# Kernel optimization log

Hardware: AMD Instinct MI355X
Metric: run time of the kernel (lower is better)

## Reference

```python
import jax, jax.numpy as jnp
import numpy as np

B, S, E, H = 1, 4096, 768, 12
D = E // H  # head_dim = 64


def setup_inputs() -> dict:
    key = jax.random.key(0)
    ks = jax.random.split(key, 6)
    scale = 0.02
    x = jax.random.normal(ks[0], (B, S, E), dtype=jnp.float32)
    Wq = jax.random.normal(ks[1], (E, E), dtype=jnp.float32) * scale
    Wk = jax.random.normal(ks[2], (E, E), dtype=jnp.float32) * scale
    Wv = jax.random.normal(ks[3], (E, E), dtype=jnp.float32) * scale
    Wo = jax.random.normal(ks[4], (E, E), dtype=jnp.float32) * scale
    bo = jax.random.normal(ks[5], (E,), dtype=jnp.float32) * scale
    mask = jnp.tril(jnp.ones((S, S), dtype=bool))[None, None]  # [1,1,S,S] causal
    return {"x": x, "Wq": Wq, "Wk": Wk, "Wv": Wv, "Wo": Wo, "bo": bo, "mask": mask}


def reference(x, Wq, Wk, Wv, Wo, bo, mask):
    # projections (torch Linear: y = x @ W.T; here W stored as [E,E] applied as x@W)
    q = jnp.einsum('bse,ef->bsf', x, Wq).reshape(B, S, H, D).transpose(0, 2, 1, 3)
    k = jnp.einsum('bse,ef->bsf', x, Wk).reshape(B, S, H, D).transpose(0, 2, 1, 3)
    v = jnp.einsum('bse,ef->bsf', x, Wv).reshape(B, S, H, D).transpose(0, 2, 1, 3)
    scores = jnp.einsum('bhqd,bhkd->bhqk', q, k) / jnp.sqrt(jnp.float32(D))
    scores = jnp.where(mask, scores, -jnp.inf)
    attn = jax.nn.softmax(scores, axis=-1)  # dropout p=0 -> identity
    ctx = jnp.einsum('bhqk,bhkd->bhqd', attn, v)
    ctx = ctx.transpose(0, 2, 1, 3).reshape(B, S, E)
    return jnp.einsum('bse,ef->bsf', ctx, Wo) + bo
```

## Files before the change

### kernel.cpp

```cpp
#include <hip/hip_runtime.h>
#include <math.h>

#define S 4096
#define E 768
#define H 12
#define Dh 64
#define SCALE2 0.1803368801111204f

typedef short short8 __attribute__((ext_vector_type(8)));
typedef float floatx4 __attribute__((ext_vector_type(4)));

__device__ __forceinline__ unsigned short f2bf(float f) {
    union { float f; unsigned int i; } c; c.f = f;
    unsigned int i = c.i;
    return (unsigned short)((i + 0x7fffu + ((i >> 16) & 1u)) >> 16);
}

__device__ __forceinline__ unsigned int pk_bf16(float lo, float hi) {
#if __has_builtin(__builtin_amdgcn_cvt_pk_bf16_f32)
    typedef __bf16 bf16x2 __attribute__((ext_vector_type(2)));
    union { bf16x2 v; unsigned int u; } c;
    c.v = __builtin_amdgcn_cvt_pk_bf16_f32(lo, hi);
    return c.u;
#else
    union { float f; unsigned int i; } a, b; a.f = lo; b.f = hi;
    return ((a.i + 0x8000u) >> 16) | ((b.i + 0x8000u) & 0xFFFF0000u);
#endif
}

__device__ __forceinline__ void gload_lds16(const unsigned short* g, unsigned short* l) {
    __builtin_amdgcn_global_load_lds(
        (const __attribute__((address_space(1))) unsigned int*)g,
        (__attribute__((address_space(3))) unsigned int*)l, 16, 0, 0);
}

__global__ __launch_bounds__(256)
void prep_kernel(const float* __restrict__ x, unsigned short* __restrict__ xb,
                 const float* __restrict__ s0, const float* __restrict__ s1,
                 const float* __restrict__ s2, const float* __restrict__ s3,
                 unsigned short* __restrict__ d0, unsigned short* __restrict__ d1,
                 unsigned short* __restrict__ d2, unsigned short* __restrict__ d3,
                 float* __restrict__ zbase) {
    __shared__ unsigned short tile[32][33];
    const int b = blockIdx.x;
    const int tid = threadIdx.x;
    if (b < 2304) {
        int z = b / 576, rem = b - z * 576;
        int bx = rem % 24, by = rem / 24;
        const float* src = (z == 0) ? s0 : (z == 1) ? s1 : (z == 2) ? s2 : s3;
        unsigned short* dst = (z == 0) ? d0 : (z == 1) ? d1 : (z == 2) ? d2 : d3;
        int tx = tid & 31, ty = tid >> 5;
        int xcol = bx * 32 + tx;
        int y0 = by * 32;
        for (int j = ty; j < 32; j += 8)
            tile[j][tx] = f2bf(src[(size_t)(y0 + j) * E + xcol]);
        __syncthreads();
        int x2 = y0 + tx;
        int y2 = bx * 32;
        for (int j = ty; j < 32; j += 8)
            dst[(size_t)(y2 + j) * E + x2] = tile[tx][j];
    } else if (b < 3840) {
        int i = ((b - 2304) * 256 + tid) * 8;
        float4 f0 = *reinterpret_cast<const float4*>(x + i);
        float4 f1 = *reinterpret_cast<const float4*>(x + i + 4);
        unsigned short u[8];
        u[0]=f2bf(f0.x); u[1]=f2bf(f0.y); u[2]=f2bf(f0.z); u[3]=f2bf(f0.w);
        u[4]=f2bf(f1.x); u[5]=f2bf(f1.y); u[6]=f2bf(f1.z); u[7]=f2bf(f1.w);
        *reinterpret_cast<uint4*>(xb + i) = *reinterpret_cast<uint4*>(u);
    } else {
        size_t i = ((size_t)(b - 3840) * 256 + tid) * 16;
        float4 z4 = make_float4(0.f, 0.f, 0.f, 0.f);
        *reinterpret_cast<float4*>(zbase + i)      = z4;
        *reinterpret_cast<float4*>(zbase + i + 4)  = z4;
        *reinterpret_cast<float4*>(zbase + i + 8)  = z4;
        *reinterpret_cast<float4*>(zbase + i + 12) = z4;
    }
}

__global__ __launch_bounds__(256)
void gemm_qkv(const unsigned short* __restrict__ A,
              const unsigned short* __restrict__ BT,
              unsigned short* __restrict__ Qb, unsigned short* __restrict__ Kb,
              unsigned short* __restrict__ VTb) {
    __shared__ unsigned short Asm[128 * 64];
    __shared__ unsigned short Bsm[128 * 64];
    const int tid  = threadIdx.x;
    const int wave = tid >> 6, lane = tid & 63;
    const int quad = lane >> 4, l16 = lane & 15;
    const int lrow = lane >> 3, lchunk = lane & 7;
    const int bb = blockIdx.x;
    const int xcd = bb & 7, j = bb >> 3;
    const int mt = (xcd >> 1) * 8 + (j & 7);
    const int nt = (xcd & 1) * 9 + (j >> 3);
    const int n0 = nt * 128;
    const int m0 = mt * 128;
    const int aw = wave >> 1, bw = wave & 1;

    floatx4 acc[4][4];
    #pragma unroll
    for (int at = 0; at < 4; at++)
        #pragma unroll
        for (int ct = 0; ct < 4; ct++)
            #pragma unroll
            for (int r = 0; r < 4; r++) acc[at][ct][r] = 0.f;

    for (int k0 = 0; k0 < E; k0 += 64) {
        #pragma unroll
        for (int i = 0; i < 4; i++) {
            int rbase = wave * 32 + i * 8;
            int row   = rbase + lrow;
            int gc    = lchunk ^ (row & 7);
            gload_lds16(&A [(size_t)(m0 + row) * E + k0 + gc * 8], &Asm[rbase * 64]);
            gload_lds16(&BT[(size_t)(n0 + row) * E + k0 + gc * 8], &Bsm[rbase * 64]);
        }
        __syncthreads();
        #pragma unroll
        for (int kk = 0; kk < 2; kk++) {
            const int g = kk * 4 + quad;
            short8 af[4], bfr[4];
            #pragma unroll
            for (int t = 0; t < 4; t++) {
                int ar = aw * 64 + t * 16 + l16;
                af[t]  = *reinterpret_cast<const short8*>(&Asm[ar * 64 + (g ^ (ar & 7)) * 8]);
                int br = bw * 64 + t * 16 + l16;
                bfr[t] = *reinterpret_cast<const short8*>(&Bsm[br * 64 + (g ^ (br & 7)) * 8]);
            }
            #pragma unroll
            for (int at = 0; at < 4; at++)
                #pragma unroll
                for (int ct = 0; ct < 4; ct++)
                    acc[at][ct] = __builtin_amdgcn_mfma_f32_16x16x32_bf16(af[at], bfr[ct], acc[at][ct], 0, 0, 0);
        }
        __syncthreads();
    }

    const int sec = n0 / 768;
    const int nb  = n0 - sec * 768 + bw * 64;
    #pragma unroll
    for (int at = 0; at < 4; at++)
        #pragma unroll
        for (int ct = 0; ct < 4; ct++) {
            int nsec = nb + ct * 16 + l16, hh = nsec >> 6, d = nsec & 63;
            #pragma unroll
            for (int r = 0; r < 4; r++) {
                int s = m0 + aw * 64 + at * 16 + quad * 4 + r;
                float v = acc[at][ct][r];
                if (sec == 0)      Qb [(size_t)hh * S * Dh + (size_t)s * Dh + d] = f2bf(v * SCALE2);
                else if (sec == 1) Kb [(size_t)hh * S * Dh + (size_t)s * Dh + d] = f2bf(v);
                else               VTb[(size_t)hh * Dh * S + (size_t)d * S + s]  = f2bf(v);
            }
        }
}

__global__ __launch_bounds__(256)
void normctx(const float* __restrict__ ctxf, const float* __restrict__ lsumf,
             unsigned short* __restrict__ ctxb) {
    int i = (blockIdx.x * 256 + threadIdx.x) * 8;
    int s = i / E, e = i - s * E;
    float linv = 1.0f / lsumf[(e >> 6) * S + s];
    float4 f0 = *reinterpret_cast<const float4*>(ctxf + i);
    float4 f1 = *reinterpret_cast<const float4*>(ctxf + i + 4);
    uint4 w;
    w.x = pk_bf16(f0.x * linv, f0.y * linv);
    w.y = pk_bf16(f0.z * linv, f0.w * linv);
    w.z = pk_bf16(f1.x * linv, f1.y * linv);
    w.w = pk_bf16(f1.z * linv, f1.w * linv);
    *reinterpret_cast<uint4*>(ctxb + i) = w;
}

__global__ __launch_bounds__(256)
void gemm_out(const unsigned short* __restrict__ A,
              const unsigned short* __restrict__ BT,
              float* __restrict__ outp, const float* __restrict__ bias) {
    __shared__ unsigned short Asm[128 * 64];
    __shared__ unsigned short Bsm[64 * 64];
    const int tid  = threadIdx.x;
    const int wave = tid >> 6, lane = tid & 63;
    const int quad = lane >> 4, l16 = lane & 15;
    const int lrow = lane >> 3, lchunk = lane & 7;
    const int bb = blockIdx.x;
    const int xcd = bb & 7, j = bb >> 3;
    const int mt = (xcd >> 1) * 8 + (j & 7);
    const int nt = (xcd & 1) * 6 + (j >> 3);
    const int n0 = nt * 64;
    const int m0 = mt * 128;

    floatx4 acc[2][4];
    #pragma unroll
    for (int at = 0; at < 2; at++)
        #pragma unroll
        for (int ct = 0; ct < 4; ct++)
            #pragma unroll
            for (int r = 0; r < 4; r++) acc[at][ct][r] = 0.f;

    for (int k0 = 0; k0 < E; k0 += 64) {
        #pragma unroll
        for (int i = 0; i < 4; i++) {
            int rbase = wave * 32 + i * 8;
            int row   = rbase + lrow;
            int gc    = lchunk ^ (row & 7);
            gload_lds16(&A[(size_t)(m0 + row) * E + k0 + gc * 8], &Asm[rbase * 64]);
        }
        #pragma unroll
        for (int i = 0; i < 2; i++) {
            int rbase = wave * 16 + i * 8;
            int row   = rbase + lrow;
            int gc    = lchunk ^ (row & 7);
            gload_lds16(&BT[(size_t)(n0 + row) * E + k0 + gc * 8], &Bsm[rbase * 64]);
        }
        __syncthreads();
        #pragma unroll
        for (int kk = 0; kk < 2; kk++) {
            const int g = kk * 4 + quad;
            short8 af[2], bfr[4];
            #pragma unroll
            for (int t = 0; t < 2; t++) {
                int ar = wave * 32 + t * 16 + l16;
                af[t] = *reinterpret_cast<const short8*>(&Asm[ar * 64 + (g ^ (ar & 7)) * 8]);
            }
            #pragma unroll
            for (int ct = 0; ct < 4; ct++) {
                int br = ct * 16 + l16;
                bfr[ct] = *reinterpret_cast<const short8*>(&Bsm[br * 64 + (g ^ (br & 7)) * 8]);
            }
            #pragma unroll
            for (int at = 0; at < 2; at++)
                #pragma unroll
                for (int ct = 0; ct < 4; ct++)
                    acc[at][ct] = __builtin_amdgcn_mfma_f32_16x16x32_bf16(af[at], bfr[ct], acc[at][ct], 0, 0, 0);
        }
        __syncthreads();
    }

    #pragma unroll
    for (int at = 0; at < 2; at++)
        #pragma unroll
        for (int ct = 0; ct < 4; ct++) {
            int n = n0 + ct * 16 + l16;
            float bn = bias[n];
            #pragma unroll
            for (int r = 0; r < 4; r++) {
                int s = m0 + wave * 32 + at * 16 + quad * 4 + r;
                outp[(size_t)s * E + n] = acc[at][ct][r] + bn;
            }
        }
}

__global__ __launch_bounds__(256)
void attn_kernel(const unsigned short* __restrict__ Q,
                 const unsigned short* __restrict__ K,
                 const unsigned short* __restrict__ VT,
                 float* __restrict__ ctxf,
                 float* __restrict__ lsumf) {
    __shared__ unsigned short Ksm[2][64 * 64];
    __shared__ unsigned short Vsm[2][64 * 64];
    __shared__ unsigned short P[4][2][16][72];
    const int tid  = threadIdx.x;
    const int wave = tid >> 6, lane = tid & 63;
    const int quad = lane >> 4, l16 = lane & 15;
    const int lrow = lane >> 3, lchunk = lane & 7;

    const int b = blockIdx.x;
    const int w = b / H;
    const int h = b - w * H;
    int Qb, ck, nck;
    if (w < 32)       { Qb = 31 - (w >> 3);       ck = w & 7;         nck = 8; }
    else if (w < 60)  { int u = w - 32;  Qb = 27 - u / 7;  ck = u % 7; nck = 7; }
    else if (w < 84)  { int u = w - 60;  Qb = 23 - u / 6;  ck = u % 6; nck = 6; }
    else if (w < 104) { int u = w - 84;  Qb = 19 - u / 5;  ck = u % 5; nck = 5; }
    else if (w < 120) { int u = w - 104; Qb = 15 - (u >> 2); ck = u & 3; nck = 4; }
    else if (w < 132) { int u = w - 120; Qb = 11 - u / 3;  ck = u % 3; nck = 3; }
    else if (w < 140) { int u = w - 132; Qb = 7 - (u >> 1); ck = u & 1; nck = 2; }
    else              { Qb = 3 - (w - 140);       ck = 0;             nck = 1; }
    const int ntiles = 2 * Qb + 2;
    const int kt0 = (ntiles * ck) / nck;
    const int kt1 = (ntiles * (ck + 1)) / nck;

    const int qs = Qb * 128 + wave * 32;

    const unsigned short* Qh = Q  + (size_t)h * S * Dh;
    const unsigned short* Kh = K  + (size_t)h * S * Dh;
    const unsigned short* Vh = VT + (size_t)h * Dh * S;

    short8 bq[2][2];
    #pragma unroll
    for (int st = 0; st < 2; st++)
        #pragma unroll
        for (int c = 0; c < 2; c++)
            bq[st][c] = *reinterpret_cast<const short8*>(
                &Qh[(size_t)(qs + st * 16 + l16) * Dh + c * 32 + quad * 8]);

    float lsum[2] = {0.f, 0.f};
    floatx4 o[2][4];
    #pragma unroll
    for (int st = 0; st < 2; st++)
        #pragma unroll
        for (int ct = 0; ct < 4; ct++)
            #pragma unroll
            for (int r = 0; r < 4; r++) o[st][ct][r] = 0.f;

    auto stage = [&](int kt, int buf) {
        #pragma unroll
        for (int i = 0; i < 2; i++) {
            int rbase = wave * 16 + i * 8;
            int row   = rbase + lrow;
            int gc    = lchunk ^ (row & 7);
            gload_lds16(&Kh[(size_t)(kt * 64 + row) * Dh + gc * 8], &Ksm[buf][rbase * 64]);
            gload_lds16(&Vh[(size_t)row * S + kt * 64 + gc * 8],    &Vsm[buf][rbase * 64]);
        }
    };

    stage(kt0, 0);
    __syncthreads();

    for (int kt = kt0; kt < kt1; kt++) {
        const int cur = (kt - kt0) & 1;
        if (kt + 1 < kt1) stage(kt + 1, cur ^ 1);

        floatx4 sc[2][4];
        #pragma unroll
        for (int st = 0; st < 2; st++)
            #pragma unroll
            for (int ct = 0; ct < 4; ct++)
                #pragma unroll
                for (int r = 0; r < 4; r++) sc[st][ct][r] = 0.f;
        #pragma unroll
        for (int c = 0; c < 2; c++)
            #pragma unroll
            for (int ct = 0; ct < 4; ct++) {
                int kr = ct * 16 + l16;
                short8 ak = *reinterpret_cast<const short8*>(
                    &Ksm[cur][kr * 64 + ((c * 4 + quad) ^ (kr & 7)) * 8]);
                sc[0][ct] = __builtin_amdgcn_mfma_f32_16x16x32_bf16(ak, bq[0][c], sc[0][ct], 0, 0, 0);
                sc[1][ct] = __builtin_amdgcn_mfma_f32_16x16x32_bf16(ak, bq[1][c], sc[1][ct], 0, 0, 0);
            }

        if (kt >= 2 * Qb) {
            #pragma unroll
            for (int st = 0; st < 2; st++) {
                int qrow = qs + st * 16 + l16;
                #pragma unroll
                for (int ct = 0; ct < 4; ct++)
                    #pragma unroll
                    for (int r = 0; r < 4; r++) {
                        int kcol = kt * 64 + ct * 16 + quad * 4 + r;
                        if (kcol > qrow) sc[st][ct][r] = -INFINITY;
                    }
            }
        }

        #pragma unroll
        for (int st = 0; st < 2; st++)
            #pragma unroll
            for (int ct = 0; ct < 4; ct++) {
                float pv[4];
                #pragma unroll
                for (int r = 0; r < 4; r++) {
                    float p = __builtin_amdgcn_exp2f(sc[st][ct][r]);
                    lsum[st] += p;
                    pv[r] = p;
                }
                uint2 w2;
                w2.x = pk_bf16(pv[0], pv[1]);
                w2.y = pk_bf16(pv[2], pv[3]);
                *reinterpret_cast<uint2*>(&P[wave][st][l16][ct * 16 + quad * 4]) = w2;
            }
        __asm__ volatile("s_waitcnt lgkmcnt(0)" ::: "memory");

        #pragma unroll
        for (int c = 0; c < 2; c++) {
            short8 ap0 = *reinterpret_cast<const short8*>(&P[wave][0][l16][c * 32 + quad * 8]);
            short8 ap1 = *reinterpret_cast<const short8*>(&P[wave][1][l16][c * 32 + quad * 8]);
            #pragma unroll
            for (int ct = 0; ct < 4; ct++) {
                int vr = ct * 16 + l16;
                short8 bv = *reinterpret_cast<const short8*>(
                    &Vsm[cur][vr * 64 + ((c * 4 + quad) ^ (vr & 7)) * 8]);
                o[0][ct] = __builtin_amdgcn_mfma_f32_16x16x32_bf16(ap0, bv, o[0][ct], 0, 0, 0);
                o[1][ct] = __builtin_amdgcn_mfma_f32_16x16x32_bf16(ap1, bv, o[1][ct], 0, 0, 0);
            }
        }
        __syncthreads();
    }

    #pragma unroll
    for (int st = 0; st < 2; st++) {
        lsum[st] += __shfl_xor(lsum[st], 16, 64);
        lsum[st] += __shfl_xor(lsum[st], 32, 64);
    }
    if (quad == 0) {
        #pragma unroll
        for (int st = 0; st < 2; st++)
            atomicAdd(&lsumf[h * S + qs + st * 16 + l16], lsum[st]);
    }
    #pragma unroll
    for (int st = 0; st < 2; st++)
        #pragma unroll
        for (int r = 0; r < 4; r++) {
            int s = qs + st * 16 + quad * 4 + r;
            #pragma unroll
            for (int ct = 0; ct < 4; ct++)
                atomicAdd(&ctxf[(size_t)s * E + h * Dh + ct * 16 + l16], o[st][ct][r]);
        }
}

extern "C" void kernel_launch(void* const* d_in, const int* in_sizes, int n_in,
                              void* d_out, int out_size, void* d_ws, size_t ws_size,
                              hipStream_t stream) {
    const float* x  = (const float*)d_in[0];
    const float* Wq = (const float*)d_in[1];
    const float* Wk = (const float*)d_in[2];
    const float* Wv = (const float*)d_in[3];
    const float* Wo = (const float*)d_in[4];
    const float* bo = (const float*)d_in[5];
    float* out = (float*)d_out;

    char* ws = (char*)d_ws;
    const size_t WT = (size_t)E * E * 2;
    const size_t QB = (size_t)S * E * 2;
    unsigned short* WqT = (unsigned short*)(ws + 0 * WT);
    unsigned short* WkT = (unsigned short*)(ws + 1 * WT);
    unsigned short* WvT = (unsigned short*)(ws + 2 * WT);
    unsigned short* WoT = (unsigned short*)(ws + 3 * WT);
    unsigned short* xb  = (unsigned short*)(ws + 4 * WT + 0 * QB);
    unsigned short* Qbf = (unsigned short*)(ws + 4 * WT + 1 * QB);
    unsigned short* Kbf = (unsigned short*)(ws + 4 * WT + 2 * QB);
    unsigned short* VTb = (unsigned short*)(ws + 4 * WT + 3 * QB);
    float*          ctxf  = (float*)(ws + 4 * WT + 4 * QB);
    float*          lsumf = (float*)(ws + 4 * WT + 4 * QB + (size_t)S * E * 4);
    unsigned short* ctxb  = (unsigned short*)(ws + 4 * WT + 4 * QB
                                              + (size_t)S * E * 4 + (size_t)H * S * 4);

    prep_kernel<<<4656, 256, 0, stream>>>(
        x, xb, Wq, Wk, Wv, Wo, WqT, WkT, WvT, WoT, ctxf);

    gemm_qkv<<<576, 256, 0, stream>>>(xb, WqT, Qbf, Kbf, VTb);

    attn_kernel<<<1728, 256, 0, stream>>>(Qbf, Kbf, VTb, ctxf, lsumf);

    normctx<<<(S * E) / (256 * 8), 256, 0, stream>>>(ctxf, lsumf, ctxb);

    gemm_out<<<384, 256, 0, stream>>>(ctxb, WoT, out, bo);
}
```

Measured before the change: 250.8 us.

## Accumulate attention context as packed bf16 atomics and fold normalization into output GEMM

The split-KV attention partials are now accumulated into a bf16 context buffer using packed bf16 atomic adds (two values per atomic) instead of fp32 atomics. The separate normalize-and-convert kernel is removed, and the softmax-denominator division is applied while the output GEMM loads its A tile into LDS. This halves atomic traffic and the zero-fill size, and drops one kernel launch plus a full read/write pass. In exchange, accumulating split chunks in bf16 loses precision, and the GEMM A tile now goes through registers rather than async global-to-LDS loads.

```diff
diff --git a/kernel.cpp b/kernel.cpp
--- a/kernel.cpp
+++ b/kernel.cpp
@@ -28,6 +28,17 @@
 #endif
 }
 
+__device__ __forceinline__ unsigned int scale_pk(unsigned int u, float s) {
+    union { unsigned int i; float f; } lo, hi;
+    lo.i = u << 16; hi.i = u & 0xffff0000u;
+    return pk_bf16(lo.f * s, hi.f * s);
+}
+
+__device__ __forceinline__ void pk_atomic_add_bf16(unsigned short* addr, unsigned int bits) {
+    unsigned long long a = (unsigned long long)addr;
+    asm volatile("global_atomic_pk_add_bf16 %0, %1, off" :: "v"(a), "v"(bits) : "memory");
+}
+
 __device__ __forceinline__ void gload_lds16(const unsigned short* g, unsigned short* l) {
     __builtin_amdgcn_global_load_lds(
         (const __attribute__((address_space(1))) unsigned int*)g,
@@ -40,7 +51,7 @@
                  const float* __restrict__ s2, const float* __restrict__ s3,
                  unsigned short* __restrict__ d0, unsigned short* __restrict__ d1,
                  unsigned short* __restrict__ d2, unsigned short* __restrict__ d3,
-                 float* __restrict__ zbase) {
+                 char* __restrict__ zbase) {
     __shared__ unsigned short tile[32][33];
     const int b = blockIdx.x;
     const int tid = threadIdx.x;
@@ -68,12 +79,12 @@
         u[4]=f2bf(f1.x); u[5]=f2bf(f1.y); u[6]=f2bf(f1.z); u[7]=f2bf(f1.w);
         *reinterpret_cast<uint4*>(xb + i) = *reinterpret_cast<uint4*>(u);
     } else {
-        size_t i = ((size_t)(b - 3840) * 256 + tid) * 16;
-        float4 z4 = make_float4(0.f, 0.f, 0.f, 0.f);
-        *reinterpret_cast<float4*>(zbase + i)      = z4;
-        *reinterpret_cast<float4*>(zbase + i + 4)  = z4;
-        *reinterpret_cast<float4*>(zbase + i + 8)  = z4;
-        *reinterpret_cast<float4*>(zbase + i + 12) = z4;
+        size_t i = (size_t)(b - 3840) * 16384 + (size_t)tid * 64;
+        uint4 z4 = make_uint4(0u, 0u, 0u, 0u);
+        *reinterpret_cast<uint4*>(zbase + i)      = z4;
+        *reinterpret_cast<uint4*>(zbase + i + 16) = z4;
+        *reinterpret_cast<uint4*>(zbase + i + 32) = z4;
+        *reinterpret_cast<uint4*>(zbase + i + 48) = z4;
     }
 }
 
@@ -153,24 +164,9 @@
 }
 
 __global__ __launch_bounds__(256)
-void normctx(const float* __restrict__ ctxf, const float* __restrict__ lsumf,
-             unsigned short* __restrict__ ctxb) {
-    int i = (blockIdx.x * 256 + threadIdx.x) * 8;
-    int s = i / E, e = i - s * E;
-    float linv = 1.0f / lsumf[(e >> 6) * S + s];
-    float4 f0 = *reinterpret_cast<const float4*>(ctxf + i);
-    float4 f1 = *reinterpret_cast<const float4*>(ctxf + i + 4);
-    uint4 w;
-    w.x = pk_bf16(f0.x * linv, f0.y * linv);
-    w.y = pk_bf16(f0.z * linv, f0.w * linv);
-    w.z = pk_bf16(f1.x * linv, f1.y * linv);
-    w.w = pk_bf16(f1.z * linv, f1.w * linv);
-    *reinterpret_cast<uint4*>(ctxb + i) = w;
-}
-
-__global__ __launch_bounds__(256)
-void gemm_out(const unsigned short* __restrict__ A,
+void gemm_out(const unsigned short* __restrict__ ctxp,
               const unsigned short* __restrict__ BT,
+              const float* __restrict__ lsumf,
               float* __restrict__ outp, const float* __restrict__ bias) {
     __shared__ unsigned short Asm[128 * 64];
     __shared__ unsigned short Bsm[64 * 64];
@@ -184,6 +180,7 @@
     const int nt = (xcd & 1) * 6 + (j >> 3);
     const int n0 = nt * 64;
     const int m0 = mt * 128;
+    const int arow = tid >> 1, ahalf = tid & 1;
 
     floatx4 acc[2][4];
     #pragma unroll
@@ -194,12 +191,20 @@
             for (int r = 0; r < 4; r++) acc[at][ct][r] = 0.f;
 
     for (int k0 = 0; k0 < E; k0 += 64) {
-        #pragma unroll
-        for (int i = 0; i < 4; i++) {
-            int rbase = wave * 32 + i * 8;
-            int row   = rbase + lrow;
-            int gc    = lchunk ^ (row & 7);
-            gload_lds16(&A[(size_t)(m0 + row) * E + k0 + gc * 8], &Asm[rbase * 64]);
+        {
+            const unsigned short* asrc = ctxp + (size_t)(m0 + arow) * E + k0 + ahalf * 32;
+            float linv = 1.0f / lsumf[(k0 >> 6) * S + m0 + arow];
+            #pragma unroll
+            for (int cc = 0; cc < 4; cc++) {
+                uint4 u = *reinterpret_cast<const uint4*>(asrc + cc * 8);
+                uint4 w;
+                w.x = scale_pk(u.x, linv);
+                w.y = scale_pk(u.y, linv);
+                w.z = scale_pk(u.z, linv);
+                w.w = scale_pk(u.w, linv);
+                int chunk = ahalf * 4 + cc;
+                *reinterpret_cast<uint4*>(&Asm[arow * 64 + (chunk ^ (arow & 7)) * 8]) = w;
+            }
         }
         #pragma unroll
         for (int i = 0; i < 2; i++) {
@@ -250,7 +255,7 @@
 void attn_kernel(const unsigned short* __restrict__ Q,
                  const unsigned short* __restrict__ K,
                  const unsigned short* __restrict__ VT,
-                 float* __restrict__ ctxf,
+                 unsigned short* __restrict__ ctxp,
                  float* __restrict__ lsumf) {
     __shared__ unsigned short Ksm[2][64 * 64];
     __shared__ unsigned short Vsm[2][64 * 64];
@@ -399,8 +404,13 @@
         for (int r = 0; r < 4; r++) {
             int s = qs + st * 16 + quad * 4 + r;
             #pragma unroll
-            for (int ct = 0; ct < 4; ct++)
-                atomicAdd(&ctxf[(size_t)s * E + h * Dh + ct * 16 + l16], o[st][ct][r]);
+            for (int ct = 0; ct < 4; ct++) {
+                float v  = o[st][ct][r];
+                float vn = __shfl_xor(v, 1, 64);
+                if ((l16 & 1) == 0)
+                    pk_atomic_add_bf16(&ctxp[(size_t)s * E + h * Dh + ct * 16 + l16],
+                                       pk_bf16(v, vn));
+            }
         }
 }
 
@@ -426,19 +436,15 @@
     unsigned short* Qbf = (unsigned short*)(ws + 4 * WT + 1 * QB);
     unsigned short* Kbf = (unsigned short*)(ws + 4 * WT + 2 * QB);
     unsigned short* VTb = (unsigned short*)(ws + 4 * WT + 3 * QB);
-    float*          ctxf  = (float*)(ws + 4 * WT + 4 * QB);
-    float*          lsumf = (float*)(ws + 4 * WT + 4 * QB + (size_t)S * E * 4);
-    unsigned short* ctxb  = (unsigned short*)(ws + 4 * WT + 4 * QB
-                                              + (size_t)S * E * 4 + (size_t)H * S * 4);
-
-    prep_kernel<<<4656, 256, 0, stream>>>(
-        x, xb, Wq, Wk, Wv, Wo, WqT, WkT, WvT, WoT, ctxf);
+    unsigned short* ctxp  = (unsigned short*)(ws + 4 * WT + 4 * QB);
+    float*          lsumf = (float*)(ws + 4 * WT + 5 * QB);
+
+    prep_kernel<<<4236, 256, 0, stream>>>(
+        x, xb, Wq, Wk, Wv, Wo, WqT, WkT, WvT, WoT, (char*)ctxp);
 
     gemm_qkv<<<576, 256, 0, stream>>>(xb, WqT, Qbf, Kbf, VTb);
 
-    attn_kernel<<<1728, 256, 0, stream>>>(Qbf, Kbf, VTb, ctxf, lsumf);
-
-    normctx<<<(S * E) / (256 * 8), 256, 0, stream>>>(ctxf, lsumf, ctxb);
-
-    gemm_out<<<384, 256, 0, stream>>>(ctxb, WoT, out, bo);
-}
+    attn_kernel<<<1728, 256, 0, stream>>>(Qbf, Kbf, VTb, ctxp, lsumf);
+
+    gemm_out<<<384, 256, 0, stream>>>(ctxp, WoT, lsumf, out, bo);
+}
```

Measured after the change: 254.0 us. No clear change (+1.3%).
